# Performance work log

Measured on AMD Instinct MI355X. Metric: run time of the kernel, lower is better.

## Reference

```python
import jax, jax.numpy as jnp
import numpy as np

# Dims: C = 8*8*4 = 256 input channels, O = 8*8*8 = 512 output channels,
# space_rank = 4, TT ranks = (4, 16, 16).

def setup_inputs() -> dict:
    key = jax.random.key(0)
    ks = jax.random.split(key, 6)
    inp = jax.random.normal(ks[0], (32, 256, 32, 32), dtype=jnp.float32)
    # space_factor: (space_rank, 1, kH, kW)
    space_factor = jax.random.normal(ks[1], (4, 1, 3, 3), dtype=jnp.float32) * 0.3
    # factors[i]: (in_i, rank_i, rank_{i+1}, out_i)
    factor0 = jax.random.normal(ks[2], (8, 4, 16, 8), dtype=jnp.float32) * 0.1
    factor1 = jax.random.normal(ks[3], (8, 16, 16, 8), dtype=jnp.float32) * 0.08
    # last_factor: (in_last, rank_last, out_last)
    last_factor = jax.random.normal(ks[4], (4, 16, 8), dtype=jnp.float32) * 0.1
    bias = jax.random.uniform(ks[5], (512,), dtype=jnp.float32, minval=-0.02, maxval=0.02)
    return {"input": inp, "space_factor": space_factor, "factor0": factor0,
            "factor1": factor1, "last_factor": last_factor, "bias": bias}


def reference(input, space_factor, factor0, factor1, last_factor, bias):
    B, C, H, W = input.shape
    sr = space_factor.shape[0]
    # Depthwise conv: each of the C channels convolved with the same
    # `space_rank` filters (torch repeat along out-channel dim + groups=C).
    w = jnp.tile(space_factor, (C, 1, 1, 1))  # (C*sr, 1, kH, kW)
    y = jax.lax.conv_general_dilated(
        input, w, window_strides=(1, 1), padding=[(1, 1), (1, 1)],
        feature_group_count=C,
        dimension_numbers=("NCHW", "OIHW", "NCHW"))  # (B, C*sr, H', W')
    Hp, Wp = y.shape[2], y.shape[3]
    # (B, n0, n1, n2, sr, H', W') with (n0,n1,n2) = input_chanel_shape
    t = y.reshape(B, 8, 8, 4, sr, Hp, Wp)
    # Contract the tiny TT cores first (optimal order found by tn.contractors.optimal):
    # chain: (n0, n1, n2, r0, o0, o1, o2) -- only ~0.5M elements.
    chain = jnp.einsum("apqx,bqry,crz->abcpxyz", factor0, factor1, last_factor)
    # One big contraction over (n0, n1, n2, r0): effectively a GEMM
    # (B*H'*W', C*sr) x (C*sr, O).
    out = jnp.einsum("nabcphw,abcpxyz->nxyzhw", t, chain)
    out = out.reshape(B, 512, Hp, Wp)
    return out + bias[None, :, None, None]
```

## Files before the change

kernel.cpp:

```cpp
#include <hip/hip_runtime.h>

typedef unsigned short ushort_t;
typedef __attribute__((ext_vector_type(8))) short bf16x8;
typedef __attribute__((ext_vector_type(8))) unsigned short ushort8;
typedef __attribute__((ext_vector_type(4))) float f32x4;

__device__ __forceinline__ unsigned short f2bf(float f) {
  union { float f; unsigned u; } x; x.f = f;
  unsigned r = x.u + 0x7FFFu + ((x.u >> 16) & 1u);
  return (unsigned short)(r >> 16);
}

__global__ __launch_bounds__(256) void chain_kernel(const float* __restrict__ f0,
                                                    const float* __restrict__ f1,
                                                    const float* __restrict__ lf,
                                                    ushort_t* __restrict__ chainT) {
  __shared__ float gs[512];
  int o = blockIdx.x;
  int z = o & 7, y = (o >> 3) & 7, x = o >> 6;
  int tid = threadIdx.x;
  #pragma unroll
  for (int i = 0; i < 2; ++i) {
    int e = tid + i * 256;
    int c = e & 3, q = (e >> 2) & 15, b = e >> 6;
    float s = 0.f;
    #pragma unroll
    for (int r = 0; r < 16; ++r)
      s += f1[((b * 16 + q) * 16 + r) * 8 + y] * lf[(c * 16 + r) * 8 + z];
    gs[e] = s;
  }
  __syncthreads();
  #pragma unroll
  for (int j = 0; j < 4; ++j) {
    int k = tid + j * 256;
    int p = k & 3, c = (k >> 2) & 3, b = (k >> 4) & 7, a = k >> 7;
    float s = 0.f;
    #pragma unroll
    for (int q = 0; q < 16; ++q)
      s += f0[((a * 4 + p) * 16 + q) * 8 + x] * gs[(b * 16 + q) * 4 + c];
    chainT[(size_t)o * 1024 + k] = f2bf(s);
  }
}

__global__ __launch_bounds__(256) void conv_kernel(const float* __restrict__ in,
                                                   const float* __restrict__ sf,
                                                   ushort_t* __restrict__ t) {
  __shared__ float in_lds[64][244];
  __shared__ float sf_l[36];
  int bid = blockIdx.x;
  int cq = bid & 3, h4 = (bid >> 2) & 7, n = bid >> 5;
  int h0 = h4 * 4;
  int tid = threadIdx.x;
  if (tid < 36) sf_l[tid] = sf[tid];
  for (int e = tid; e < 384; e += 256) {
    int ch = e / 6, r = e % 6;
    in_lds[ch][r * 40 + 3] = 0.f;
    in_lds[ch][r * 40 + 36] = 0.f;
  }
  const float* inb = in + ((size_t)n * 256 + cq * 64) * 1024;
  #pragma unroll
  for (int i = 0; i < 12; ++i) {
    int e = tid + i * 256;
    int ch = e / 48, rem = e % 48;
    int r = rem >> 3, w4 = rem & 7;
    int hh = h0 - 1 + r;
    float4 v = make_float4(0.f, 0.f, 0.f, 0.f);
    if (hh >= 0 && hh < 32)
      v = *(const float4*)&inb[(size_t)ch * 1024 + hh * 32 + w4 * 4];
    *(float4*)&in_lds[ch][r * 40 + 4 + w4 * 4] = v;
  }
  __syncthreads();
  float sfr[36];
  #pragma unroll
  for (int i = 0; i < 36; ++i) sfr[i] = sf_l[i];
  int w = tid >> 3, gg = tid & 7;
  size_t m0 = (size_t)n * 1024 + (size_t)h0 * 32 + w;
  #pragma unroll
  for (int j = 0; j < 4; ++j) {
    float acc[4][2][4];
    #pragma unroll
    for (int b = 0; b < 2; ++b) {
      int ch = j * 16 + gg * 2 + b;
      float vals[6][3];
      #pragma unroll
      for (int r = 0; r < 6; ++r)
        #pragma unroll
        for (int dw = 0; dw < 3; ++dw)
          vals[r][dw] = in_lds[ch][r * 40 + 3 + w + dw];
      #pragma unroll
      for (int hh = 0; hh < 4; ++hh)
        #pragma unroll
        for (int p = 0; p < 4; ++p) {
          float s = 0.f;
          #pragma unroll
          for (int dr = 0; dr < 3; ++dr)
            #pragma unroll
            for (int dw = 0; dw < 3; ++dw)
              s += vals[hh + dr][dw] * sfr[p * 9 + dr * 3 + dw];
          acc[hh][b][p] = s;
        }
    }
    #pragma unroll
    for (int hh = 0; hh < 4; ++hh) {
      ushort8 outv;
      #pragma unroll
      for (int b = 0; b < 2; ++b)
        #pragma unroll
        for (int p = 0; p < 4; ++p) outv[b * 4 + p] = f2bf(acc[hh][b][p]);
      *(ushort8*)&t[(m0 + hh * 32) * 1024 + (size_t)(cq * 256 + j * 64 + gg * 8)] = outv;
    }
  }
}

#define AS1 __attribute__((address_space(1)))
#define AS3 __attribute__((address_space(3)))
#define BARRIER  __builtin_amdgcn_s_barrier()
#define VMCNT3   asm volatile("s_waitcnt vmcnt(3)" ::: "memory")
#define VMCNT0   asm volatile("s_waitcnt vmcnt(0)" ::: "memory")

__global__ __launch_bounds__(512, 4) void gemm_kernel(const ushort_t* __restrict__ tA,
                                                      const ushort_t* __restrict__ tB,
                                                      const float* __restrict__ bias,
                                                      float* __restrict__ out) {
  __shared__ __align__(16) ushort_t As[3][8192];
  __shared__ __align__(16) ushort_t Bs[3][4096];
  int tid = threadIdx.x;
  int bid = blockIdx.x;
  int wg = (bid & 7) * 64 + (bid >> 3);
  int tile_m = (wg >> 2) * 256;
  int tile_n = (wg & 3) * 128;

  int lane = tid & 63, wv = tid >> 6;
  int wm2 = (wv >> 2) * 128, wn4 = (wv & 3) * 32;
  int lr = lane & 15, kg = lane >> 4;
  int kph = ((kg ^ (lr & 3)) * 8);

  int srow = tid >> 2;
  int lsw = (tid & 3) ^ (srow & 3);
  const ushort_t* sA = tA + (size_t)(tile_m + srow) * 1024 + lsw * 8;
  const ushort_t* sB = tB + (size_t)(tile_n + srow) * 1024 + lsw * 8;

#define STAGE(SB, KT)                                                                    \
  __builtin_amdgcn_global_load_lds((const AS1 void*)(sA + (KT) * 32),                    \
      (AS3 void*)&As[SB][tid * 8], 16, 0, 0);                                            \
  __builtin_amdgcn_global_load_lds((const AS1 void*)(sA + 131072 + (KT) * 32),           \
      (AS3 void*)&As[SB][4096 + tid * 8], 16, 0, 0);                                     \
  __builtin_amdgcn_global_load_lds((const AS1 void*)(sB + (KT) * 32),                    \
      (AS3 void*)&Bs[SB][tid * 8], 16, 0, 0);

#define COMPUTE(BUF)                                                                     \
  {                                                                                      \
    bf16x8 af[8], bq[2];                                                                 \
    _Pragma("unroll")                                                                    \
    for (int mf = 0; mf < 8; ++mf)                                                       \
      af[mf] = *(const bf16x8*)&As[BUF][(wm2 + mf * 16 + lr) * 32 + kph];                \
    _Pragma("unroll")                                                                    \
    for (int nf = 0; nf < 2; ++nf)                                                       \
      bq[nf] = *(const bf16x8*)&Bs[BUF][(wn4 + nf * 16 + lr) * 32 + kph];                \
    __builtin_amdgcn_s_setprio(1);                                                       \
    _Pragma("unroll")                                                                    \
    for (int mf = 0; mf < 8; ++mf)                                                       \
      _Pragma("unroll")                                                                  \
      for (int nf = 0; nf < 2; ++nf)                                                     \
        acc[mf][nf] = __builtin_amdgcn_mfma_f32_16x16x32_bf16(                           \
            af[mf], bq[nf], acc[mf][nf], 0, 0, 0);                                       \
    __builtin_amdgcn_s_setprio(0);                                                       \
  }

  f32x4 acc[8][2];
  #pragma unroll
  for (int i = 0; i < 8; ++i)
    #pragma unroll
    for (int j = 0; j < 2; ++j) acc[i][j] = (f32x4){0.f, 0.f, 0.f, 0.f};

  float bv[2];
  #pragma unroll
  for (int nf = 0; nf < 2; ++nf) bv[nf] = bias[tile_n + wn4 + nf * 16 + lr];

  STAGE(0, 0) STAGE(1, 1)
  VMCNT3; BARRIER;

  #pragma unroll 1
  for (int I = 0; I < 10; ++I) {
    int kt = 3 * I;
    STAGE(2, kt + 2)
    COMPUTE(0)
    VMCNT3; BARRIER;
    STAGE(0, kt + 3)
    COMPUTE(1)
    VMCNT3; BARRIER;
    STAGE(1, kt + 4)
    COMPUTE(2)
    VMCNT3; BARRIER;
  }
  COMPUTE(0)
  VMCNT0; BARRIER;
  COMPUTE(1)

  #pragma unroll
  for (int mf = 0; mf < 8; ++mf)
    #pragma unroll
    for (int nf = 0; nf < 2; ++nf) {
      int m = tile_m + wm2 + mf * 16 + kg * 4;
      int o = tile_n + wn4 + nf * 16 + lr;
      f32x4 v = acc[mf][nf];
      v[0] += bv[nf]; v[1] += bv[nf]; v[2] += bv[nf]; v[3] += bv[nf];
      *(f32x4*)&out[(size_t)(m >> 10) * 524288 + (size_t)o * 1024 + (size_t)(m & 1023)] = v;
    }
}

extern "C" void kernel_launch(void* const* d_in, const int* in_sizes, int n_in,
                              void* d_out, int out_size, void* d_ws, size_t ws_size,
                              hipStream_t stream) {
  (void)in_sizes; (void)n_in; (void)out_size; (void)ws_size;
  const float* in   = (const float*)d_in[0];
  const float* sf   = (const float*)d_in[1];
  const float* f0   = (const float*)d_in[2];
  const float* f1   = (const float*)d_in[3];
  const float* lf   = (const float*)d_in[4];
  const float* bias = (const float*)d_in[5];
  float* out = (float*)d_out;

  char* ws = (char*)d_ws;
  ushort_t* t      = (ushort_t*)ws;
  ushort_t* chainT = (ushort_t*)(ws + 67108864);

  hipLaunchKernelGGL(chain_kernel, dim3(512),  dim3(256), 0, stream, f0, f1, lf, chainT);
  hipLaunchKernelGGL(conv_kernel,  dim3(1024), dim3(256), 0, stream, in, sf, t);
  hipLaunchKernelGGL(gemm_kernel,  dim3(512),  dim3(512), 0, stream, t, chainT, bias, out);
}
```

Before: 80.88 us.

## Retile depthwise conv to 16-channel 8-row blocks and square GEMM warp tiles

The conv kernel now handles 16 channels by 8 rows per block across 2048 blocks instead of 64 channels by 4 rows. Each thread computes 8 output rows for two channels from a 10-row register window, so fewer halo rows are reloaded, and it packs the bf16 pairs into uint4 stores. The GEMM changes the per-wave tile from 128x32 to 64x64, which reduces redundant LDS fragment reads per MFMA from 10 to 8 per 16. The LDS swizzle is adjusted to match the new layout. Bias is now loaded inside the epilogue instead of being hoisted.

Measured after the change: 75.43 us. -6.7%, faster.

```diff
diff --git a/kernel.cpp b/kernel.cpp
--- a/kernel.cpp
+++ b/kernel.cpp
@@ -45,23 +45,22 @@
 __global__ __launch_bounds__(256) void conv_kernel(const float* __restrict__ in,
                                                    const float* __restrict__ sf,
                                                    ushort_t* __restrict__ t) {
-  __shared__ float in_lds[64][244];
+  __shared__ float in_lds[16][404];
   __shared__ float sf_l[36];
   int bid = blockIdx.x;
-  int cq = bid & 3, h4 = (bid >> 2) & 7, n = bid >> 5;
-  int h0 = h4 * 4;
+  int cg = bid & 15, hg = (bid >> 4) & 3, n = bid >> 6;
+  int h0 = hg * 8;
   int tid = threadIdx.x;
   if (tid < 36) sf_l[tid] = sf[tid];
-  for (int e = tid; e < 384; e += 256) {
-    int ch = e / 6, r = e % 6;
-    in_lds[ch][r * 40 + 3] = 0.f;
-    in_lds[ch][r * 40 + 36] = 0.f;
-  }
-  const float* inb = in + ((size_t)n * 256 + cq * 64) * 1024;
-  #pragma unroll
-  for (int i = 0; i < 12; ++i) {
+  for (int e = tid; e < 320; e += 256) {
+    int ch = e / 20, rr = e % 20;
+    in_lds[ch][(rr >> 1) * 40 + 3 + (rr & 1) * 33] = 0.f;
+  }
+  const float* inb = in + ((size_t)n * 256 + cg * 16) * 1024;
+  #pragma unroll
+  for (int i = 0; i < 5; ++i) {
     int e = tid + i * 256;
-    int ch = e / 48, rem = e % 48;
+    int ch = e / 80, rem = e % 80;
     int r = rem >> 3, w4 = rem & 7;
     int hh = h0 - 1 + r;
     float4 v = make_float4(0.f, 0.f, 0.f, 0.f);
@@ -73,42 +72,39 @@
   float sfr[36];
   #pragma unroll
   for (int i = 0; i < 36; ++i) sfr[i] = sf_l[i];
-  int w = tid >> 3, gg = tid & 7;
+  int w = tid & 31, sub = tid >> 5;
   size_t m0 = (size_t)n * 1024 + (size_t)h0 * 32 + w;
-  #pragma unroll
-  for (int j = 0; j < 4; ++j) {
-    float acc[4][2][4];
-    #pragma unroll
-    for (int b = 0; b < 2; ++b) {
-      int ch = j * 16 + gg * 2 + b;
-      float vals[6][3];
+  unsigned pw[8][4];
+  #pragma unroll
+  for (int b = 0; b < 2; ++b) {
+    int ch = sub * 2 + b;
+    float vals[10][3];
+    #pragma unroll
+    for (int r = 0; r < 10; ++r)
       #pragma unroll
-      for (int r = 0; r < 6; ++r)
+      for (int dw = 0; dw < 3; ++dw)
+        vals[r][dw] = in_lds[ch][r * 40 + 3 + w + dw];
+    #pragma unroll
+    for (int j = 0; j < 8; ++j) {
+      float s0 = 0.f, s1 = 0.f, s2 = 0.f, s3 = 0.f;
+      #pragma unroll
+      for (int dr = 0; dr < 3; ++dr)
         #pragma unroll
-        for (int dw = 0; dw < 3; ++dw)
-          vals[r][dw] = in_lds[ch][r * 40 + 3 + w + dw];
-      #pragma unroll
-      for (int hh = 0; hh < 4; ++hh)
-        #pragma unroll
-        for (int p = 0; p < 4; ++p) {
-          float s = 0.f;
-          #pragma unroll
-          for (int dr = 0; dr < 3; ++dr)
-            #pragma unroll
-            for (int dw = 0; dw < 3; ++dw)
-              s += vals[hh + dr][dw] * sfr[p * 9 + dr * 3 + dw];
-          acc[hh][b][p] = s;
+        for (int dw = 0; dw < 3; ++dw) {
+          float tv = vals[j + dr][dw];
+          s0 += tv * sfr[0 * 9 + dr * 3 + dw];
+          s1 += tv * sfr[1 * 9 + dr * 3 + dw];
+          s2 += tv * sfr[2 * 9 + dr * 3 + dw];
+          s3 += tv * sfr[3 * 9 + dr * 3 + dw];
         }
+      pw[j][b * 2 + 0] = (unsigned)f2bf(s0) | ((unsigned)f2bf(s1) << 16);
+      pw[j][b * 2 + 1] = (unsigned)f2bf(s2) | ((unsigned)f2bf(s3) << 16);
     }
-    #pragma unroll
-    for (int hh = 0; hh < 4; ++hh) {
-      ushort8 outv;
-      #pragma unroll
-      for (int b = 0; b < 2; ++b)
-        #pragma unroll
-        for (int p = 0; p < 4; ++p) outv[b * 4 + p] = f2bf(acc[hh][b][p]);
-      *(ushort8*)&t[(m0 + hh * 32) * 1024 + (size_t)(cq * 256 + j * 64 + gg * 8)] = outv;
-    }
+  }
+  #pragma unroll
+  for (int j = 0; j < 8; ++j) {
+    uint4 pk; pk.x = pw[j][0]; pk.y = pw[j][1]; pk.z = pw[j][2]; pk.w = pw[j][3];
+    *(uint4*)&t[(m0 + (size_t)j * 32) * 1024 + (size_t)(cg * 64 + sub * 8)] = pk;
   }
 }
 
@@ -131,12 +127,12 @@
   int tile_n = (wg & 3) * 128;
 
   int lane = tid & 63, wv = tid >> 6;
-  int wm2 = (wv >> 2) * 128, wn4 = (wv & 3) * 32;
+  int wm = (wv >> 1) * 64, wn = (wv & 1) * 64;
   int lr = lane & 15, kg = lane >> 4;
-  int kph = ((kg ^ (lr & 3)) * 8);
+  int kph = ((kg ^ ((lr >> 1) & 3)) * 8);
 
   int srow = tid >> 2;
-  int lsw = (tid & 3) ^ (srow & 3);
+  int lsw = (tid & 3) ^ ((srow >> 1) & 3);
   const ushort_t* sA = tA + (size_t)(tile_m + srow) * 1024 + lsw * 8;
   const ushort_t* sB = tB + (size_t)(tile_n + srow) * 1024 + lsw * 8;
 
@@ -150,32 +146,28 @@
 
 #define COMPUTE(BUF)                                                                     \
   {                                                                                      \
-    bf16x8 af[8], bq[2];                                                                 \
+    bf16x8 af[4], bq[4];                                                                 \
     _Pragma("unroll")                                                                    \
-    for (int mf = 0; mf < 8; ++mf)                                                       \
-      af[mf] = *(const bf16x8*)&As[BUF][(wm2 + mf * 16 + lr) * 32 + kph];                \
+    for (int mf = 0; mf < 4; ++mf)                                                       \
+      af[mf] = *(const bf16x8*)&As[BUF][(wm + mf * 16 + lr) * 32 + kph];                 \
     _Pragma("unroll")                                                                    \
-    for (int nf = 0; nf < 2; ++nf)                                                       \
-      bq[nf] = *(const bf16x8*)&Bs[BUF][(wn4 + nf * 16 + lr) * 32 + kph];                \
+    for (int nf = 0; nf < 4; ++nf)                                                       \
+      bq[nf] = *(const bf16x8*)&Bs[BUF][(wn + nf * 16 + lr) * 32 + kph];                 \
     __builtin_amdgcn_s_setprio(1);                                                       \
     _Pragma("unroll")                                                                    \
-    for (int mf = 0; mf < 8; ++mf)                                                       \
+    for (int mf = 0; mf < 4; ++mf)                                                       \
       _Pragma("unroll")                                                                  \
-      for (int nf = 0; nf < 2; ++nf)                                                     \
+      for (int nf = 0; nf < 4; ++nf)                                                     \
         acc[mf][nf] = __builtin_amdgcn_mfma_f32_16x16x32_bf16(                           \
             af[mf], bq[nf], acc[mf][nf], 0, 0, 0);                                       \
     __builtin_amdgcn_s_setprio(0);                                                       \
   }
 
-  f32x4 acc[8][2];
-  #pragma unroll
-  for (int i = 0; i < 8; ++i)
-    #pragma unroll
-    for (int j = 0; j < 2; ++j) acc[i][j] = (f32x4){0.f, 0.f, 0.f, 0.f};
-
-  float bv[2];
-  #pragma unroll
-  for (int nf = 0; nf < 2; ++nf) bv[nf] = bias[tile_n + wn4 + nf * 16 + lr];
+  f32x4 acc[4][4];
+  #pragma unroll
+  for (int i = 0; i < 4; ++i)
+    #pragma unroll
+    for (int j = 0; j < 4; ++j) acc[i][j] = (f32x4){0.f, 0.f, 0.f, 0.f};
 
   STAGE(0, 0) STAGE(1, 1)
   VMCNT3; BARRIER;
@@ -198,13 +190,14 @@
   COMPUTE(1)
 
   #pragma unroll
-  for (int mf = 0; mf < 8; ++mf)
-    #pragma unroll
-    for (int nf = 0; nf < 2; ++nf) {
-      int m = tile_m + wm2 + mf * 16 + kg * 4;
-      int o = tile_n + wn4 + nf * 16 + lr;
+  for (int mf = 0; mf < 4; ++mf)
+    #pragma unroll
+    for (int nf = 0; nf < 4; ++nf) {
+      int m = tile_m + wm + mf * 16 + kg * 4;
+      int o = tile_n + wn + nf * 16 + lr;
+      float bv = bias[o];
       f32x4 v = acc[mf][nf];
-      v[0] += bv[nf]; v[1] += bv[nf]; v[2] += bv[nf]; v[3] += bv[nf];
+      v[0] += bv; v[1] += bv; v[2] += bv; v[3] += bv;
       *(f32x4*)&out[(size_t)(m >> 10) * 524288 + (size_t)o * 1024 + (size_t)(m & 1023)] = v;
     }
 }
@@ -226,6 +219,6 @@
   ushort_t* chainT = (ushort_t*)(ws + 67108864);
 
   hipLaunchKernelGGL(chain_kernel, dim3(512),  dim3(256), 0, stream, f0, f1, lf, chainT);
-  hipLaunchKernelGGL(conv_kernel,  dim3(1024), dim3(256), 0, stream, in, sf, t);
+  hipLaunchKernelGGL(conv_kernel,  dim3(2048), dim3(256), 0, stream, in, sf, t);
   hipLaunchKernelGGL(gemm_kernel,  dim3(512),  dim3(512), 0, stream, t, chainT, bias, out);
 }
```
